# Kernel tuning notes

Measured on AMD Instinct MI355X. Metric: run time of the kernel, lower is better.

## Reference

```python
import jax, jax.numpy as jnp
import numpy as np

H = 1024


def setup_inputs() -> dict:
    key = jax.random.key(0)
    ks = jax.random.split(key, 8)
    B, S = 32, 2048
    query = jax.random.normal(ks[0], (B, 1, H), dtype=jnp.float32)
    keys = jax.random.normal(ks[1], (B, S, H), dtype=jnp.float32)
    s = 1.0 / np.sqrt(H)
    Wa_w = jax.random.uniform(ks[2], (H, H), jnp.float32, -s, s)
    Wa_b = jax.random.uniform(ks[3], (H,), jnp.float32, -s, s)
    Ua_w = jax.random.uniform(ks[4], (H, H), jnp.float32, -s, s)
    Ua_b = jax.random.uniform(ks[5], (H,), jnp.float32, -s, s)
    Va_w = jax.random.uniform(ks[6], (1, H), jnp.float32, -s, s)
    Va_b = jax.random.uniform(ks[7], (1,), jnp.float32, -s, s)
    return {"query": query, "keys": keys, "Wa_w": Wa_w, "Wa_b": Wa_b,
            "Ua_w": Ua_w, "Ua_b": Ua_b, "Va_w": Va_w, "Va_b": Va_b}


def reference(query, keys, Wa_w, Wa_b, Ua_w, Ua_b, Va_w, Va_b):
    # query: [B,1,H]; keys: [B,S,H]
    q_proj = jnp.einsum('boh,kh->bok', query, Wa_w) + Wa_b      # [B,1,H], broadcasts over S
    k_proj = jnp.einsum('bsh,kh->bsk', keys, Ua_w) + Ua_b       # [B,S,H]
    e = jnp.tanh(q_proj + k_proj)                               # [B,S,H]
    scores = jnp.einsum('bsh,h->bs', e, Va_w[0]) + Va_b[0]      # [B,S]
    weights = jax.nn.softmax(scores, axis=1)[:, None, :]        # [B,1,S]
    context = jnp.einsum('bos,bsh->boh', weights, keys)         # [B,1,H]
    return (context, weights)
```

## Files before the change

kernel.cpp:

```cpp
#include <hip/hip_runtime.h>
#include <hip/hip_bf16.h>

#define H 1024
#define B 32
#define S 2048

typedef __attribute__((ext_vector_type(8))) short bf16x8;
typedef __attribute__((ext_vector_type(4))) float f32x4;

union U4 { uint4 u; bf16x8 b; };

__device__ __forceinline__ unsigned short f2bf(float f) {
    unsigned u = __float_as_uint(f);
    unsigned r = (u + 0x7fffu + ((u >> 16) & 1u)) >> 16;
    return (unsigned short)r;
}

__device__ __forceinline__ uint4 pack8(float4 x, float4 y) {
    uint4 p;
    p.x = (unsigned)f2bf(x.x) | ((unsigned)f2bf(x.y) << 16);
    p.y = (unsigned)f2bf(x.z) | ((unsigned)f2bf(x.w) << 16);
    p.z = (unsigned)f2bf(y.x) | ((unsigned)f2bf(y.y) << 16);
    p.w = (unsigned)f2bf(y.z) | ((unsigned)f2bf(y.w) << 16);
    return p;
}

__device__ __forceinline__ float ftanh(float x) {
    float x2 = __builtin_amdgcn_fmed3f(x + x, -30.f, 30.f);
    float e = __expf(x2);
    return 1.f - 2.f * __builtin_amdgcn_rcpf(e + 1.f);
}

__device__ __forceinline__ void async_copy16(const void* g, void* l) {
    __builtin_amdgcn_global_load_lds(
        (const __attribute__((address_space(1))) unsigned int*)g,
        (__attribute__((address_space(3))) unsigned int*)l, 16, 0, 0);
}

__global__ void k0_swizzle(const float* __restrict__ Ua, uint4* __restrict__ UaSw) {
    int t = blockIdx.x * 256 + threadIdx.x;
    int lane = t & 63;
    int nt = (t >> 6) & 7;
    int kc = (t >> 9) & 31;
    int nb = t >> 14;
    int n = nb * 128 + nt * 16 + (lane & 15);
    int k = kc * 32 + ((lane >> 4) & 3) * 8;
    const float4* src = (const float4*)(Ua + (size_t)n * H + k);
    UaSw[t] = pack8(src[0], src[1]);
}

__global__ __launch_bounds__(256) void ka_swz(const float* __restrict__ keys,
                                              uint4* __restrict__ Abf) {
    size_t g = (size_t)blockIdx.x * 256 + threadIdx.x;
    int lane = (int)(g & 63);
    size_t u = g >> 6;
    int kc = (int)(u & 31);
    size_t stile = u >> 5;
    size_t row = stile * 16 + (lane & 15);
    int col = kc * 32 + ((lane >> 4) & 3) * 8;
    const float4* src = (const float4*)(keys + row * H + col);
    Abf[g] = pack8(src[0], src[1]);
}

__global__ __launch_bounds__(256) void k1_qproj(
    const float* __restrict__ q, const float* __restrict__ Wa,
    const float* __restrict__ Wab, const float* __restrict__ Uab,
    float* __restrict__ qp) {
    int b = blockIdx.y;
    int t = threadIdx.x;
    int n = blockIdx.x * 64 + (t >> 2);
    int quarter = t & 3;
    __shared__ float qs[H];
    for (int i = t; i < H; i += 256) qs[i] = q[b * H + i];
    __syncthreads();
    const float4* wr = (const float4*)(Wa + (size_t)n * H + quarter * 256);
    const float* qq = qs + quarter * 256;
    float acc = 0.f;
#pragma unroll 4
    for (int i = 0; i < 64; i++) {
        float4 w = wr[i];
        acc += qq[i * 4 + 0] * w.x + qq[i * 4 + 1] * w.y +
               qq[i * 4 + 2] * w.z + qq[i * 4 + 3] * w.w;
    }
    acc += __shfl_xor(acc, 1, 64);
    acc += __shfl_xor(acc, 2, 64);
    if (quarter == 0) qp[b * H + n] = acc + Wab[n] + Uab[n];
}

__global__ __launch_bounds__(256, 2) void k2_scores2(
    const uint4* __restrict__ Abf, const uint4* __restrict__ UaSw,
    const float* __restrict__ qp, const float* __restrict__ Vaw,
    float* __restrict__ sp) {
    const int tid = threadIdx.x;
    const int lane = tid & 63;
    const int wm = tid >> 6;
    const int lid = blockIdx.x;
    const int c = lid & 7;
    const int qq = lid >> 3;
    const int nb = qq & 7;
    const int mb = (qq >> 3) * 8 + c;
    const int b = mb >> 4;
    const int s0 = (mb & 15) << 7;

    const int stile0 = mb * 8 + wm * 2;
    const uint4* pa = Abf + (size_t)stile0 * 2048 + lane;
    const uint4* pb = UaSw + (size_t)nb * 16384 + lane;

    f32x4 acc[2][8];
#pragma unroll
    for (int mt = 0; mt < 2; mt++)
#pragma unroll
        for (int nt = 0; nt < 8; nt++) acc[mt][nt] = (f32x4){0.f, 0.f, 0.f, 0.f};

    U4 fa[4][2], fb[4][8];
#pragma unroll
    for (int p = 0; p < 4; p++) {
        fa[p][0].u = pa[p * 64];
        fa[p][1].u = pa[p * 64 + 2048];
#pragma unroll
        for (int nt = 0; nt < 8; nt++) fb[p][nt].u = pb[p * 512 + nt * 64];
    }

    for (int kc = 0; kc < 32; kc += 4) {
#pragma unroll
        for (int p = 0; p < 4; p++) {
#pragma unroll
            for (int nt = 0; nt < 8; nt++)
#pragma unroll
                for (int mt = 0; mt < 2; mt++)
                    acc[mt][nt] = __builtin_amdgcn_mfma_f32_16x16x32_bf16(
                        fa[p][mt].b, fb[p][nt].b, acc[mt][nt], 0, 0, 0);
            const int kn = (kc + 4 + p) & 31;
            fa[p][0].u = pa[kn * 64];
            fa[p][1].u = pa[kn * 64 + 2048];
#pragma unroll
            for (int nt = 0; nt < 8; nt++) fb[p][nt].u = pb[kn * 512 + nt * 64];
        }
    }

    const int col = lane & 15, qd = lane >> 4;
    float qv[8], vv[8];
#pragma unroll
    for (int nt = 0; nt < 8; nt++) {
        int n = nb * 128 + nt * 16 + col;
        qv[nt] = qp[b * H + n];
        vv[nt] = Vaw[n];
    }
#pragma unroll
    for (int mt = 0; mt < 2; mt++) {
        float rs[4] = {0.f, 0.f, 0.f, 0.f};
#pragma unroll
        for (int nt = 0; nt < 8; nt++)
#pragma unroll
            for (int r = 0; r < 4; r++)
                rs[r] += ftanh(acc[mt][nt][r] + qv[nt]) * vv[nt];
#pragma unroll
        for (int r = 0; r < 4; r++) {
            float v = rs[r];
            v += __shfl_xor(v, 1, 64);
            v += __shfl_xor(v, 2, 64);
            v += __shfl_xor(v, 4, 64);
            v += __shfl_xor(v, 8, 64);
            if (col == 0)
                sp[(size_t)nb * B * S + b * S + s0 + wm * 32 + mt * 16 + qd * 4 + r] = v;
        }
    }
}

__global__ __launch_bounds__(256) void k4_ctx2(const uint4* __restrict__ Abf,
                                               const float* __restrict__ sp,
                                               float* __restrict__ out) {
    int kcg = blockIdx.x, b = blockIdx.y;
    int t = threadIdx.x;
    __shared__ float red[256];
    __shared__ float wl[S];

    float v[8];
#pragma unroll
    for (int i = 0; i < 8; i++) {
        int s = i * 256 + t;
        float sum = 0.f;
#pragma unroll
        for (int nb = 0; nb < 8; nb++) sum += sp[(size_t)nb * B * S + b * S + s];
        v[i] = sum;
    }
    float lm = -1e30f;
#pragma unroll
    for (int i = 0; i < 8; i++) lm = fmaxf(lm, v[i]);
    red[t] = lm;
    __syncthreads();
    for (int s = 128; s > 0; s >>= 1) {
        if (t < s) red[t] = fmaxf(red[t], red[t + s]);
        __syncthreads();
    }
    float m = red[0];
    __syncthreads();
    float ls = 0.f;
#pragma unroll
    for (int i = 0; i < 8; i++) ls += __expf(v[i] - m);
    red[t] = ls;
    __syncthreads();
    for (int s = 128; s > 0; s >>= 1) {
        if (t < s) red[t] += red[t + s];
        __syncthreads();
    }
    float inv = 1.f / red[0];
#pragma unroll
    for (int i = 0; i < 8; i++) {
        int s = i * 256 + t;
        float w = __expf(v[i] - m) * inv;
        wl[s] = w;
        if (kcg == 0) out[B * H + b * S + s] = w;
    }
    __syncthreads();

    const int wv = t >> 6, lane = t & 63, qd = lane >> 4, colr = lane & 15;
    const int kc = kcg * 4 + wv;
    float a8[8] = {0.f, 0.f, 0.f, 0.f, 0.f, 0.f, 0.f, 0.f};
    const uint4* base = Abf + ((size_t)(b * 128) * 32 + kc) * 64 + lane;
#pragma unroll 4
    for (int st = 0; st < 128; st++) {
        uint4 f = base[(size_t)st * 2048];
        float w = wl[st * 16 + colr];
        a8[0] += w * __uint_as_float(f.x << 16);
        a8[1] += w * __uint_as_float(f.x & 0xffff0000u);
        a8[2] += w * __uint_as_float(f.y << 16);
        a8[3] += w * __uint_as_float(f.y & 0xffff0000u);
        a8[4] += w * __uint_as_float(f.z << 16);
        a8[5] += w * __uint_as_float(f.z & 0xffff0000u);
        a8[6] += w * __uint_as_float(f.w << 16);
        a8[7] += w * __uint_as_float(f.w & 0xffff0000u);
    }
#pragma unroll
    for (int j = 0; j < 8; j++) {
        float vj = a8[j];
        vj += __shfl_xor(vj, 1, 64);
        vj += __shfl_xor(vj, 2, 64);
        vj += __shfl_xor(vj, 4, 64);
        vj += __shfl_xor(vj, 8, 64);
        a8[j] = vj;
    }
    if (colr == 0) {
        int colbase = kc * 32 + qd * 8;
#pragma unroll
        for (int j = 0; j < 8; j++) out[b * H + colbase + j] = a8[j];
    }
}

__global__ __launch_bounds__(256, 3) void k2_scores_fb(
    const float* __restrict__ keys, const uint4* __restrict__ UaSw,
    const float* __restrict__ qp, const float* __restrict__ Vaw,
    float* __restrict__ sp) {
    __shared__ uint4 As[2][512];
    __shared__ uint4 Bs[2][512];
    __shared__ float part[2][128];
    const int tid = threadIdx.x;
    const int lane = tid & 63;
    const int wave = tid >> 6;
    const int wm = wave >> 1, wn = wave & 1;
    const int lid = blockIdx.x;
    const int c = lid & 7;
    const int qq = lid >> 3;
    const int nb = qq & 7;
    const int mb = (qq >> 3) * 8 + c;
    const int b = mb >> 4;
    const int s0 = (mb & 15) << 7;
    const int el = tid & 63;
    const int srow0 = s0 + (tid >> 6) * 16 + (el & 15);
    const int srow1 = srow0 + 64;
    const int kofs = ((el >> 4) & 3) * 8;
    const float4* ka0 = (const float4*)(keys + ((size_t)b * S + srow0) * H + kofs);
    const float4* ka1 = (const float4*)(keys + ((size_t)b * S + srow1) * H + kofs);
    const uint4* srcB = UaSw + (size_t)nb * 32 * 512;
    f32x4 acc[4][4];
#pragma unroll
    for (int mt = 0; mt < 4; mt++)
#pragma unroll
        for (int nt = 0; nt < 4; nt++) acc[mt][nt] = (f32x4){0.f, 0.f, 0.f, 0.f};
    float4 x0 = ka0[0], y0 = ka0[1], x1 = ka1[0], y1 = ka1[1];
    async_copy16(srcB + tid,       &Bs[0][tid]);
    async_copy16(srcB + tid + 256, &Bs[0][tid + 256]);
    As[0][tid]       = pack8(x0, y0);
    As[0][tid + 256] = pack8(x1, y1);
    x0 = ka0[8]; y0 = ka0[9]; x1 = ka1[8]; y1 = ka1[9];
    __syncthreads();
    for (int kc = 0; kc < 32; kc++) {
        const int cur = kc & 1, nxt = cur ^ 1;
        if (kc < 31) {
            async_copy16(srcB + (size_t)(kc + 1) * 512 + tid,       &Bs[nxt][tid]);
            async_copy16(srcB + (size_t)(kc + 1) * 512 + tid + 256, &Bs[nxt][tid + 256]);
            As[nxt][tid]       = pack8(x0, y0);
            As[nxt][tid + 256] = pack8(x1, y1);
            if (kc < 30) {
                x0 = ka0[(kc + 2) * 8]; y0 = ka0[(kc + 2) * 8 + 1];
                x1 = ka1[(kc + 2) * 8]; y1 = ka1[(kc + 2) * 8 + 1];
            }
        }
        U4 af[4], bf[4];
#pragma unroll
        for (int mt = 0; mt < 4; mt++) af[mt].u = As[cur][(wm * 4 + mt) * 64 + lane];
#pragma unroll
        for (int nt = 0; nt < 4; nt++) bf[nt].u = Bs[cur][(wn * 4 + nt) * 64 + lane];
#pragma unroll
        for (int mt = 0; mt < 4; mt++)
#pragma unroll
            for (int nt = 0; nt < 4; nt++)
                acc[mt][nt] = __builtin_amdgcn_mfma_f32_16x16x32_bf16(
                    af[mt].b, bf[nt].b, acc[mt][nt], 0, 0, 0);
        __syncthreads();
    }
    const int col = lane & 15, qd = lane >> 4;
    float qv[4], vv[4];
#pragma unroll
    for (int nt = 0; nt < 4; nt++) {
        int n = nb * 128 + (wn * 4 + nt) * 16 + col;
        qv[nt] = qp[b * H + n];
        vv[nt] = Vaw[n];
    }
#pragma unroll
    for (int mt = 0; mt < 4; mt++) {
        float rs[4] = {0.f, 0.f, 0.f, 0.f};
#pragma unroll
        for (int nt = 0; nt < 4; nt++)
#pragma unroll
            for (int r = 0; r < 4; r++)
                rs[r] += ftanh(acc[mt][nt][r] + qv[nt]) * vv[nt];
#pragma unroll
        for (int r = 0; r < 4; r++) {
            float v = rs[r];
            v += __shfl_xor(v, 1, 64);
            v += __shfl_xor(v, 2, 64);
            v += __shfl_xor(v, 4, 64);
            v += __shfl_xor(v, 8, 64);
            if (col == 0) part[wn][wm * 64 + mt * 16 + qd * 4 + r] = v;
        }
    }
    __syncthreads();
    if (tid < 128)
        sp[(size_t)nb * B * S + b * S + s0 + tid] = part[0][tid] + part[1][tid];
}

__global__ __launch_bounds__(256) void k4_ctx_fb(const float* __restrict__ keys,
                                                 const float* __restrict__ sp,
                                                 float* __restrict__ out) {
    int sc = blockIdx.x, b = blockIdx.y;
    int t = threadIdx.x;
    __shared__ float red[256];
    __shared__ float wl[64];
    float v[8];
#pragma unroll
    for (int i = 0; i < 8; i++) {
        int s = i * 256 + t;
        float sum = 0.f;
#pragma unroll
        for (int nb = 0; nb < 8; nb++) sum += sp[(size_t)nb * B * S + b * S + s];
        v[i] = sum;
    }
    float lm = -1e30f;
#pragma unroll
    for (int i = 0; i < 8; i++) lm = fmaxf(lm, v[i]);
    red[t] = lm;
    __syncthreads();
    for (int s = 128; s > 0; s >>= 1) {
        if (t < s) red[t] = fmaxf(red[t], red[t + s]);
        __syncthreads();
    }
    float m = red[0];
    __syncthreads();
    float ls = 0.f;
#pragma unroll
    for (int i = 0; i < 8; i++) ls += __expf(v[i] - m);
    red[t] = ls;
    __syncthreads();
    for (int s = 128; s > 0; s >>= 1) {
        if (t < s) red[t] += red[t + s];
        __syncthreads();
    }
    float inv = 1.f / red[0];
    if (t < 64) {
        int s = sc * 64 + t;
        float sum = 0.f;
#pragma unroll
        for (int nb = 0; nb < 8; nb++) sum += sp[(size_t)nb * B * S + b * S + s];
        float w = __expf(sum - m) * inv;
        wl[t] = w;
        out[B * H + b * S + s] = w;
    }
    __syncthreads();
    const float4* kp = (const float4*)(keys + ((size_t)b * S + sc * 64) * H) + t;
    float4 acc = {0.f, 0.f, 0.f, 0.f};
#pragma unroll 8
    for (int s = 0; s < 64; s++) {
        float4 kv = kp[(size_t)s * 256];
        float w = wl[s];
        acc.x += w * kv.x; acc.y += w * kv.y;
        acc.z += w * kv.z; acc.w += w * kv.w;
    }
    float* dst = out + b * H + t * 4;
    atomicAdd(dst + 0, acc.x);
    atomicAdd(dst + 1, acc.y);
    atomicAdd(dst + 2, acc.z);
    atomicAdd(dst + 3, acc.w);
}

extern "C" void kernel_launch(void* const* d_in, const int* in_sizes, int n_in,
                              void* d_out, int out_size, void* d_ws, size_t ws_size,
                              hipStream_t stream) {
    const float* query = (const float*)d_in[0];
    const float* keys  = (const float*)d_in[1];
    const float* Wa_w  = (const float*)d_in[2];
    const float* Wa_b  = (const float*)d_in[3];
    const float* Ua_w  = (const float*)d_in[4];
    const float* Ua_b  = (const float*)d_in[5];
    const float* Va_w  = (const float*)d_in[6];
    float* out = (float*)d_out;

    uint4* UaSw = (uint4*)d_ws;
    float* qp = (float*)((char*)d_ws + (2u << 20));
    float* sp = (float*)((char*)d_ws + (2u << 20) + (128u << 10));
    uint4* Abf = (uint4*)((char*)d_ws + (8u << 20));
    const size_t NEED = (size_t)(8u << 20) + ((size_t)128u << 20);

    if (ws_size >= NEED) {
        ka_swz<<<32768, 256, 0, stream>>>(keys, Abf);
        k0_swizzle<<<512, 256, 0, stream>>>(Ua_w, UaSw);
        k1_qproj<<<dim3(16, B), 256, 0, stream>>>(query, Wa_w, Wa_b, Ua_b, qp);
        k2_scores2<<<4096, 256, 0, stream>>>(Abf, UaSw, qp, Va_w, sp);
        k4_ctx2<<<dim3(8, B), 256, 0, stream>>>(Abf, sp, out);
    } else {
        hipMemsetAsync(d_out, 0, B * H * sizeof(float), stream);
        k0_swizzle<<<512, 256, 0, stream>>>(Ua_w, UaSw);
        k1_qproj<<<dim3(16, B), 256, 0, stream>>>(query, Wa_w, Wa_b, Ua_b, qp);
        k2_scores_fb<<<4096, 256, 0, stream>>>(keys, UaSw, qp, Va_w, sp);
        k4_ctx_fb<<<dim3(32, B), 256, 0, stream>>>(keys, sp, out);
    }
}
```

Baseline: 619.0 us.

## Restructure score GEMM into 256x256 LDS tiles with 4-stage async copy pipeline

Replaces the register-direct scores GEMM with a 512-thread block computing a 256x256 tile. Operands are staged into LDS through 4-stage async global-to-LDS copies, and 8 waves share the A and B fragments. This raises operand reuse and cuts global/L2 traffic per MFMA, while the pipelined loads hide latency and setprio favours the MFMA waves. It needs 128KB of dynamic LDS, which limits occupancy. The partial-score planes grow from 8 to 16, so the context kernel sums more planes.

```diff
diff --git a/kernel.cpp b/kernel.cpp
--- a/kernel.cpp
+++ b/kernel.cpp
@@ -87,70 +87,102 @@
     if (quarter == 0) qp[b * H + n] = acc + Wab[n] + Uab[n];
 }
 
-__global__ __launch_bounds__(256, 2) void k2_scores2(
+__global__ __launch_bounds__(512, 2) void k2_scores3(
     const uint4* __restrict__ Abf, const uint4* __restrict__ UaSw,
     const float* __restrict__ qp, const float* __restrict__ Vaw,
     float* __restrict__ sp) {
+    extern __shared__ uint4 bufs[];
     const int tid = threadIdx.x;
     const int lane = tid & 63;
-    const int wm = tid >> 6;
+    const int w = tid >> 6;
+    const int wm = w >> 2;
+    const int wn = w & 3;
+
     const int lid = blockIdx.x;
     const int c = lid & 7;
-    const int qq = lid >> 3;
-    const int nb = qq & 7;
-    const int mb = (qq >> 3) * 8 + c;
-    const int b = mb >> 4;
-    const int s0 = (mb & 15) << 7;
-
-    const int stile0 = mb * 8 + wm * 2;
-    const uint4* pa = Abf + (size_t)stile0 * 2048 + lane;
-    const uint4* pb = UaSw + (size_t)nb * 16384 + lane;
-
-    f32x4 acc[2][8];
-#pragma unroll
-    for (int mt = 0; mt < 2; mt++)
-#pragma unroll
-        for (int nt = 0; nt < 8; nt++) acc[mt][nt] = (f32x4){0.f, 0.f, 0.f, 0.f};
-
-    U4 fa[4][2], fb[4][8];
-#pragma unroll
-    for (int p = 0; p < 4; p++) {
-        fa[p][0].u = pa[p * 64];
-        fa[p][1].u = pa[p * 64 + 2048];
-#pragma unroll
-        for (int nt = 0; nt < 8; nt++) fb[p][nt].u = pb[p * 512 + nt * 64];
-    }
-
-    for (int kc = 0; kc < 32; kc += 4) {
-#pragma unroll
-        for (int p = 0; p < 4; p++) {
-#pragma unroll
-            for (int nt = 0; nt < 8; nt++)
-#pragma unroll
-                for (int mt = 0; mt < 2; mt++)
-                    acc[mt][nt] = __builtin_amdgcn_mfma_f32_16x16x32_bf16(
-                        fa[p][mt].b, fb[p][nt].b, acc[mt][nt], 0, 0, 0);
-            const int kn = (kc + 4 + p) & 31;
-            fa[p][0].u = pa[kn * 64];
-            fa[p][1].u = pa[kn * 64 + 2048];
-#pragma unroll
-            for (int nt = 0; nt < 8; nt++) fb[p][nt].u = pb[kn * 512 + nt * 64];
+    const int qidx = lid >> 3;
+    const int nblk = qidx & 3;
+    const int mb = (qidx >> 2) * 8 + c;
+    const int b = mb >> 3;
+    const int stile0 = mb * 16;
+
+    f32x4 acc[8][4];
+#pragma unroll
+    for (int mt = 0; mt < 8; mt++)
+#pragma unroll
+        for (int nt = 0; nt < 4; nt++) acc[mt][nt] = (f32x4){0.f, 0.f, 0.f, 0.f};
+
+    auto STAGE = [&](int kt, int tb) {
+        uint4* dst = bufs + tb * 2048;
+        if (w < 4) {
+#pragma unroll
+            for (int i = 0; i < 4; i++) {
+                int st = w * 4 + i;
+                async_copy16(Abf + ((size_t)(stile0 + st) * 32 + kt) * 64 + lane,
+                             dst + st * 64 + lane);
+            }
+        } else {
+#pragma unroll
+            for (int i = 0; i < 4; i++) {
+                int nt = (w - 4) * 4 + i;
+                int nbu = nblk * 2 + (nt >> 3);
+                async_copy16(UaSw + (size_t)nbu * 16384 + (size_t)kt * 512 +
+                                 (nt & 7) * 64 + lane,
+                             dst + 1024 + nt * 64 + lane);
+            }
         }
+    };
+
+    STAGE(0, 0);
+    __builtin_amdgcn_sched_barrier(0);
+    STAGE(1, 1);
+    __builtin_amdgcn_sched_barrier(0);
+    STAGE(2, 2);
+    __builtin_amdgcn_sched_barrier(0);
+    asm volatile("s_waitcnt vmcnt(8)" ::: "memory");
+    __builtin_amdgcn_s_barrier();
+    __builtin_amdgcn_sched_barrier(0);
+
+#pragma unroll 4
+    for (int t = 0; t < 32; t++) {
+        STAGE((t + 3) & 31, (t + 3) & 3);
+
+        const uint4* cur = bufs + (t & 3) * 2048;
+        U4 a[8], bb[4];
+#pragma unroll
+        for (int mt = 0; mt < 8; mt++) a[mt].u = cur[(wm * 8 + mt) * 64 + lane];
+#pragma unroll
+        for (int nt = 0; nt < 4; nt++) bb[nt].u = cur[1024 + (wn * 4 + nt) * 64 + lane];
+
+        __builtin_amdgcn_s_setprio(1);
+#pragma unroll
+        for (int mt = 0; mt < 8; mt++)
+#pragma unroll
+            for (int nt = 0; nt < 4; nt++)
+                acc[mt][nt] = __builtin_amdgcn_mfma_f32_16x16x32_bf16(
+                    a[mt].b, bb[nt].b, acc[mt][nt], 0, 0, 0);
+        __builtin_amdgcn_s_setprio(0);
+
+        __builtin_amdgcn_sched_barrier(0);
+        asm volatile("s_waitcnt vmcnt(8)" ::: "memory");
+        __builtin_amdgcn_s_barrier();
+        __builtin_amdgcn_sched_barrier(0);
     }
 
     const int col = lane & 15, qd = lane >> 4;
-    float qv[8], vv[8];
-#pragma unroll
-    for (int nt = 0; nt < 8; nt++) {
-        int n = nb * 128 + nt * 16 + col;
+    float qv[4], vv[4];
+#pragma unroll
+    for (int nt = 0; nt < 4; nt++) {
+        int n = nblk * 256 + (wn * 4 + nt) * 16 + col;
         qv[nt] = qp[b * H + n];
         vv[nt] = Vaw[n];
     }
-#pragma unroll
-    for (int mt = 0; mt < 2; mt++) {
+    const int plane = nblk * 4 + wn;
+#pragma unroll
+    for (int mt = 0; mt < 8; mt++) {
         float rs[4] = {0.f, 0.f, 0.f, 0.f};
 #pragma unroll
-        for (int nt = 0; nt < 8; nt++)
+        for (int nt = 0; nt < 4; nt++)
 #pragma unroll
             for (int r = 0; r < 4; r++)
                 rs[r] += ftanh(acc[mt][nt][r] + qv[nt]) * vv[nt];
@@ -162,7 +194,8 @@
             v += __shfl_xor(v, 4, 64);
             v += __shfl_xor(v, 8, 64);
             if (col == 0)
-                sp[(size_t)nb * B * S + b * S + s0 + wm * 32 + mt * 16 + qd * 4 + r] = v;
+                sp[(size_t)plane * (B * S) + mb * 256 +
+                   (wm * 8 + mt) * 16 + qd * 4 + r] = v;
         }
     }
 }
@@ -181,7 +214,7 @@
         int s = i * 256 + t;
         float sum = 0.f;
 #pragma unroll
-        for (int nb = 0; nb < 8; nb++) sum += sp[(size_t)nb * B * S + b * S + s];
+        for (int nb = 0; nb < 16; nb++) sum += sp[(size_t)nb * B * S + b * S + s];
         v[i] = sum;
     }
     float lm = -1e30f;
@@ -422,10 +455,16 @@
     const size_t NEED = (size_t)(8u << 20) + ((size_t)128u << 20);
 
     if (ws_size >= NEED) {
+        static bool inited = false;
+        if (!inited) {
+            hipFuncSetAttribute(reinterpret_cast<const void*>(k2_scores3),
+                                hipFuncAttributeMaxDynamicSharedMemorySize, 131072);
+            inited = true;
+        }
         ka_swz<<<32768, 256, 0, stream>>>(keys, Abf);
         k0_swizzle<<<512, 256, 0, stream>>>(Ua_w, UaSw);
         k1_qproj<<<dim3(16, B), 256, 0, stream>>>(query, Wa_w, Wa_b, Ua_b, qp);
-        k2_scores2<<<4096, 256, 0, stream>>>(Abf, UaSw, qp, Va_w, sp);
+        k2_scores3<<<1024, 512, 131072, stream>>>(Abf, UaSw, qp, Va_w, sp);
         k4_ctx2<<<dim3(8, B), 256, 0, stream>>>(Abf, sp, out);
     } else {
         hipMemsetAsync(d_out, 0, B * H * sizeof(float), stream);
```

Result: slower. 749.0 us (+21.0%).
